# Performance work log

Measured on AMD Instinct MI355X. Metric: run time of the kernel, lower is better.

The kernel has to match this reference:

```python
import jax, jax.numpy as jnp
import numpy as np
import math

B, H, L = 8, 256, 4096
C = 1            # channels
D_STATE = 64
DD = D_STATE // 2  # d = 32
DT_MIN, DT_MAX = 1e-3, 1e-1


def setup_inputs() -> dict:
    key = jax.random.key(0)
    ks = jax.random.split(key, 6)
    u = jax.random.normal(ks[0], (B, H, L), dtype=jnp.float32)
    # analytic init matching the torch module
    h_scale = jnp.exp(jnp.arange(H, dtype=jnp.float32) / H * math.log(DT_MAX / DT_MIN))  # (H,)
    angles = jnp.arange(DD, dtype=jnp.float32) * jnp.float32(np.pi)                      # (DD,)
    theta = jnp.einsum('c,h,d->chd', jnp.ones((C,), jnp.float32), h_scale, angles)       # (C,H,DD)
    a = -jnp.broadcast_to(h_scale[None, :, None], (C, H, DD)).astype(jnp.float32)        # (C,H,DD)
    D = jax.random.normal(ks[1], (C, H), dtype=jnp.float32)
    b_p = jax.random.normal(ks[2], (C, H, DD), dtype=jnp.float32)
    c_p = jax.random.normal(ks[3], (C, H, DD), dtype=jnp.float32)
    x0 = jax.random.normal(ks[4], (C, H, DD), dtype=jnp.float32)
    return {"u": u, "theta": theta, "a": a, "D": D, "b_p": b_p, "c_p": c_p, "x0": x0}


def fft_conv(u, f):
    # u: (B,H,L), f: (C,H,L) -> (B,C,H,L) causal conv via zero-padded FFT
    l = u.shape[-1]
    n = 2 * l
    u_f = jnp.fft.rfft(u, n=n)          # (B,H,n//2+1)
    f_f = jnp.fft.rfft(f, n=n)          # (C,H,n//2+1)
    y_f = jnp.einsum('bhl,chl->bchl', u_f, f_f)
    return jnp.fft.irfft(y_f, n=n)[..., :l]


def reference(u, theta, a, D, b_p, c_p, x0):
    l = u.shape[-1]
    T = 1.0 / (l - 1)
    zk = T * jnp.arange(l, dtype=jnp.float32)            # (L,)
    zk4 = zk[None, None, :, None]                         # (1,1,L,1)
    ls = -jnp.abs(a) + 1j * theta                         # (C,H,DD) complex
    term_0 = (jnp.exp(ls * T) - 1.0) / ls                 # (C,H,DD)
    # base_term: (C,H,L,DD)
    base_term = (2.0 * term_0[:, :, None, :] * jnp.exp(ls[:, :, None, :] * zk4)).real
    q = b_p * c_p                                         # (C,H,DD)
    f = jnp.einsum('chd,chld->chl', q, base_term)         # (C,H,L)
    y = fft_conv(u, f)                                    # (B,C,H,L)
    y = y + jnp.einsum('bhl,ch->bchl', u, D)
    # initial-condition term
    cos_term = 2.0 * T * jnp.exp(-jnp.abs(a)[:, :, None, :] * zk4) * jnp.cos(theta[:, :, None, :] * zk4)
    init = jnp.einsum('chd,chld->chl', 2.0 * (c_p * x0), cos_term)  # (C,H,L)
    y = y + init[None]                                    # broadcast over batch
    b = y.shape[0]
    return y.reshape(b, -1, l)                            # (B, C*H, L)
```

## Files before the change

kernel.cpp:

```cpp
#include <hip/hip_runtime.h>

#define BB 8
#define HH 256
#define LL 4096
#define STR 72

typedef __attribute__((ext_vector_type(8))) short short8;
typedef __attribute__((ext_vector_type(4))) float f32x4;

static __device__ inline unsigned short f2bf(float x) {
    union { float f; unsigned u; } v; v.f = x;
    unsigned r = v.u + 0x7fffu + ((v.u >> 16) & 1u);
    return (unsigned short)(r >> 16);
}
static __device__ inline float bf2f(unsigned short us) {
    union { unsigned u; float f; } v; v.u = ((unsigned)us) << 16; return v.f;
}

#define CMUL(or_, oi_, ar_, ai_, br_, bi_) do { \
    float _tr = fmaf((ar_), (br_), -(ai_) * (bi_)); \
    float _ti = fmaf((ar_), (bi_), (ai_) * (br_)); \
    (or_) = _tr; (oi_) = _ti; } while (0)

__global__ __launch_bounds__(256, 4) void s4_fused_kernel(
    const float* __restrict__ u, const float* __restrict__ theta,
    const float* __restrict__ a, const float* __restrict__ Dp,
    const float* __restrict__ b_p, const float* __restrict__ c_p,
    const float* __restrict__ x0, float* __restrict__ out)
{
    const int tid = threadIdx.x;
    const int blk = blockIdx.x;
    const int hh  = blk >> 2;
    const int bp  = blk & 3;

    __shared__ __align__(16) short UsA[64 * STR];
    __shared__ __align__(16) short UsB[64 * STR];
    __shared__ __align__(16) short EQ[64 * STR];
    __shared__ __align__(16) float Seg[32 * 18];
    __shared__ float h_s[64];

    const int d    = tid & 31;
    const int kb   = tid >> 5;
    const int g    = tid >> 5;
    const int ln   = tid & 63;
    const int m0   = (tid >> 6) << 4;
    const int rowi = ln & 15;
    const int quad = ln >> 4;

    const float* up0 = u + ((((size_t)(bp * 2) * HH) + hh) << 12);
    const float* up1 = u + ((((size_t)(bp * 2 + 1) * HH) + hh) << 12);
    float4 v0[4];
    #pragma unroll
    for (int jj = 0; jj < 4; ++jj)
        v0[jj] = ((const float4*)up0)[tid + (jj << 8)];

    const float T = 1.0f / (LL - 1);
    const float lr = a[hh * 32 + d];
    const float li = theta[hh * 32 + d];
    float sn, cS;
    sincosf(li * T, &sn, &cS);
    const float er = expf(lr * T);
    const float Rr = er * cS, Ri = er * sn;
    const float den = lr * lr + li * li;
    const float t0r = ((Rr - 1.f) * lr + Ri * li) / den;
    const float t0i = (Ri * lr - (Rr - 1.f) * li) / den;
    const float qq  = b_p[hh * 32 + d] * c_p[hh * 32 + d];
    const float wre = 2.f * qq * t0r, wim = 2.f * qq * t0i;
    const float vv  = 4.f * T * c_p[hh * 32 + d] * x0[hh * 32 + d];
    const float Dh  = Dp[hh];

    float r2r, r2i, r4r, r4i, r8r, r8i, r16r, r16i, r32r, r32i;
    CMUL(r2r, r2i, Rr, Ri, Rr, Ri);
    CMUL(r4r, r4i, r2r, r2i, r2r, r2i);
    CMUL(r8r, r8i, r4r, r4i, r4r, r4i);
    CMUL(r16r, r16i, r8r, r8i, r8r, r8i);
    CMUL(r32r, r32i, r16r, r16i, r16r, r16i);

    {
        float pr = 1.f, pi = 0.f;
        if (kb & 1) CMUL(pr, pi, pr, pi, r8r, r8i);
        if (kb & 2) CMUL(pr, pi, pr, pi, r16r, r16i);
        if (kb & 4) CMUL(pr, pi, pr, pi, r32r, r32i);
        #pragma unroll
        for (int k8 = 0; k8 < 8; ++k8) {
            const int k = (kb << 3) + k8;
            EQ[k * STR + d]            = (short)f2bf(pr);
            EQ[k * STR + 32 + d]       = (short)f2bf(-pi);
            UsB[d * STR + (63 - k)]        = (short)f2bf(pr);
            UsB[(32 + d) * STR + (63 - k)] = (short)f2bf(pi);
            float hk = fmaf(wre, pr, -wim * pi);
            hk += __shfl_xor(hk, 1);
            hk += __shfl_xor(hk, 2);
            hk += __shfl_xor(hk, 4);
            hk += __shfl_xor(hk, 8);
            hk += __shfl_xor(hk, 16);
            if (d == 0) h_s[k] = hk;
            CMUL(pr, pi, pr, pi, Rr, Ri);
        }
    }

    float Ar, Ai, wrr, wri;
    CMUL(Ar, Ai, r32r, r32i, r32r, r32i);
    CMUL(wrr, wri, wre, wim, Rr, Ri);
    float S8r, S8i, S16r, S16i, S32r, S32i;
    {
        float b1r, b1i, b2r, b2i;
        CMUL(b1r, b1i, Ar, Ai, Ar, Ai);
        CMUL(b2r, b2i, b1r, b1i, b1r, b1i);
        CMUL(S8r, S8i, b2r, b2i, b2r, b2i);
        CMUL(S16r, S16i, S8r, S8i, S8r, S8i);
        CMUL(S32r, S32i, S16r, S16i, S16r, S16i);
    }
    __syncthreads();

    {
        const int t  = tid >> 2;
        const int tb = (tid & 3) << 4;
        #pragma unroll
        for (int gg = 0; gg < 4; ++gg) {
            const int tau0 = tb + (gg << 2);
            unsigned short e[4];
            #pragma unroll
            for (int i = 0; i < 4; ++i) {
                const int dt = t - (tau0 + i);
                e[i] = (dt >= 0) ? f2bf(h_s[dt]) : (unsigned short)0;
            }
            uint2 pk;
            pk.x = (unsigned)e[0] | ((unsigned)e[1] << 16);
            pk.y = (unsigned)e[2] | ((unsigned)e[3] << 16);
            *(uint2*)&UsA[t * STR + tau0] = pk;
        }
    }
    __syncthreads();

    short8 aH[2], aP[2], aR[2];
    #pragma unroll
    for (int kh = 0; kh < 2; ++kh) {
        const int off = (m0 + rowi) * STR + (kh << 5) + (quad << 3);
        aH[kh] = *(const short8*)&UsA[off];
        aP[kh] = *(const short8*)&UsB[off];
        aR[kh] = *(const short8*)&EQ[off];
    }
    __syncthreads();

    #pragma unroll
    for (int jj = 0; jj < 4; ++jj) {
        const int v  = tid + (jj << 8);
        const int c  = v >> 4;
        const int t0 = (v & 15) << 2;
        uint2 pk;
        pk.x = (unsigned)f2bf(v0[jj].x) | ((unsigned)f2bf(v0[jj].y) << 16);
        pk.y = (unsigned)f2bf(v0[jj].z) | ((unsigned)f2bf(v0[jj].w) << 16);
        *(uint2*)&UsA[c * STR + t0] = pk;
    }
    float4 v1[4];
    #pragma unroll
    for (int jj = 0; jj < 4; ++jj)
        v1[jj] = ((const float4*)up1)[tid + (jj << 8)];
    __syncthreads();

    #pragma unroll
    for (int it = 0; it < 2; ++it) {
        short* Us = it ? UsB : UsA;

        f32x4 accY[4], accE[4];
        #pragma unroll
        for (int nt = 0; nt < 4; ++nt) {
            accY[nt] = (f32x4){0.f, 0.f, 0.f, 0.f};
            accE[nt] = (f32x4){0.f, 0.f, 0.f, 0.f};
        }
        #pragma unroll
        for (int kh = 0; kh < 2; ++kh) {
            const int k0 = kh << 5;
            #pragma unroll
            for (int nt = 0; nt < 4; ++nt) {
                const short8 bU = *(const short8*)&Us[((nt << 4) + rowi) * STR + k0 + (quad << 3)];
                accY[nt] = __builtin_amdgcn_mfma_f32_16x16x32_bf16(aH[kh], bU, accY[nt], 0, 0, 0);
                accE[nt] = __builtin_amdgcn_mfma_f32_16x16x32_bf16(aP[kh], bU, accE[nt], 0, 0, 0);
            }
        }

        #pragma unroll
        for (int nt = 0; nt < 4; ++nt) {
            uint2 pk;
            pk.x = (unsigned)f2bf(accE[nt][0]) | ((unsigned)f2bf(accE[nt][1]) << 16);
            pk.y = (unsigned)f2bf(accE[nt][2]) | ((unsigned)f2bf(accE[nt][3]) << 16);
            *(uint2*)&EQ[((nt << 4) + rowi) * STR + m0 + (quad << 2)] = pk;
        }

        if (it == 0) {
            #pragma unroll
            for (int jj = 0; jj < 4; ++jj) {
                const int v  = tid + (jj << 8);
                const int c  = v >> 4;
                const int t0 = (v & 15) << 2;
                uint2 pk;
                pk.x = (unsigned)f2bf(v1[jj].x) | ((unsigned)f2bf(v1[jj].y) << 16);
                pk.y = (unsigned)f2bf(v1[jj].z) | ((unsigned)f2bf(v1[jj].w) << 16);
                *(uint2*)&UsB[c * STR + t0] = pk;
            }
        }
        __syncthreads();

        const int cb = g << 3;
        float Er[8], Ei[8];
        {
            float Sr = 0.f, Si = 0.f;
            #pragma unroll
            for (int i = 0; i < 8; ++i) {
                const int c = cb + i;
                Er[i] = bf2f((unsigned short)EQ[c * STR + d]);
                Ei[i] = bf2f((unsigned short)EQ[c * STR + 32 + d]);
                const float nr = fmaf(Ar, Sr, fmaf(-Ai, Si, Er[i]));
                const float ni = fmaf(Ar, Si, fmaf(Ai, Sr, Ei[i]));
                Sr = nr; Si = ni;
            }
            Seg[d * 18 + (g << 1)]     = Sr;
            Seg[d * 18 + (g << 1) + 1] = Si;
        }
        __syncthreads();

        {
            float offr = 0.f, offi = 0.f;
            #pragma unroll
            for (int gp = 0; gp < 7; ++gp) {
                const float2 sg = *(const float2*)&Seg[d * 18 + (gp << 1)];
                const float nr = fmaf(S8r, offr, fmaf(-S8i, offi, sg.x));
                const float ni = fmaf(S8r, offi, fmaf(S8i, offr, sg.y));
                const bool take = gp < g;
                offr = take ? nr : offr;
                offi = take ? ni : offi;
            }
            float Gr = vv, Gi = 0.f;
            if (g & 1) { float nr, ni; CMUL(nr, ni, Gr, Gi, S8r, S8i);   Gr = nr; Gi = ni; }
            if (g & 2) { float nr, ni; CMUL(nr, ni, Gr, Gi, S16r, S16i); Gr = nr; Gi = ni; }
            if (g & 4) { float nr, ni; CMUL(nr, ni, Gr, Gi, S32r, S32i); Gr = nr; Gi = ni; }
            float Sr = offr, Si = offi;
            #pragma unroll
            for (int i = 0; i < 8; ++i) {
                const int c = cb + i;
                const float Qr = fmaf(wrr, Sr, fmaf(-wri, Si, Gr));
                const float Qi = fmaf(wrr, Si, fmaf(wri, Sr, Gi));
                EQ[c * STR + d]      = (short)f2bf(Qr);
                EQ[c * STR + 32 + d] = (short)f2bf(Qi);
                const float nr = fmaf(Ar, Sr, fmaf(-Ai, Si, Er[i]));
                const float ni = fmaf(Ar, Si, fmaf(Ai, Sr, Ei[i]));
                Sr = nr; Si = ni;
                float nGr, nGi;
                CMUL(nGr, nGi, Ar, Ai, Gr, Gi);
                Gr = nGr; Gi = nGi;
            }
        }
        __syncthreads();

        #pragma unroll
        for (int kh = 0; kh < 2; ++kh) {
            const int k0 = kh << 5;
            #pragma unroll
            for (int nt = 0; nt < 4; ++nt) {
                const short8 bQ = *(const short8*)&EQ[((nt << 4) + rowi) * STR + k0 + (quad << 3)];
                accY[nt] = __builtin_amdgcn_mfma_f32_16x16x32_bf16(aR[kh], bQ, accY[nt], 0, 0, 0);
            }
        }

        float* op = out + ((((size_t)(bp * 2 + it) * HH) + hh) << 12);
        #pragma unroll
        for (int nt = 0; nt < 4; ++nt) {
            const int c    = (nt << 4) + rowi;
            const int toff = m0 + (quad << 2);
            const uint2 uu = *(const uint2*)&Us[c * STR + toff];
            float4 res;
            res.x = fmaf(Dh, bf2f((unsigned short)(uu.x & 0xffffu)), accY[nt][0]);
            res.y = fmaf(Dh, bf2f((unsigned short)(uu.x >> 16)),     accY[nt][1]);
            res.z = fmaf(Dh, bf2f((unsigned short)(uu.y & 0xffffu)), accY[nt][2]);
            res.w = fmaf(Dh, bf2f((unsigned short)(uu.y >> 16)),     accY[nt][3]);
            *(float4*)&op[c * 64 + toff] = res;
        }
        __syncthreads();
    }
}

extern "C" void kernel_launch(void* const* d_in, const int* in_sizes, int n_in,
                              void* d_out, int out_size, void* d_ws, size_t ws_size,
                              hipStream_t stream) {
    const float* u     = (const float*)d_in[0];
    const float* theta = (const float*)d_in[1];
    const float* a     = (const float*)d_in[2];
    const float* Dp    = (const float*)d_in[3];
    const float* b_p   = (const float*)d_in[4];
    const float* c_p   = (const float*)d_in[5];
    const float* x0    = (const float*)d_in[6];
    float* out = (float*)d_out;
    (void)d_ws; (void)ws_size;

    hipLaunchKernelGGL(s4_fused_kernel, dim3(HH * 4), dim3(256), 0, stream,
                       u, theta, a, Dp, b_p, c_p, x0, out);
}
```

Baseline: 101.7 us.

## Assign one batch per block and build Toeplitz fragment directly in registers

The grid grows from 1024 blocks handling two batches each to 2048 blocks handling one batch each. This removes the per-block loop and the second u prefetch. The Toeplitz A-fragment is now built in registers from a bf16 h vector kept in shared memory, rather than staged through a shared-memory matrix, which drops one LDS pass and two barriers. In exchange, each block still recomputes the per-h setup (powers, P and R matrices), so that setup work doubles across the grid, and the in-block overlap of the next batch's load goes away.

```diff
diff --git a/kernel.cpp b/kernel.cpp
--- a/kernel.cpp
+++ b/kernel.cpp
@@ -30,14 +30,14 @@
 {
     const int tid = threadIdx.x;
     const int blk = blockIdx.x;
-    const int hh  = blk >> 2;
-    const int bp  = blk & 3;
-
-    __shared__ __align__(16) short UsA[64 * STR];
-    __shared__ __align__(16) short UsB[64 * STR];
+    const int hh  = blk >> 3;
+    const int b   = blk & 7;
+
+    __shared__ __align__(16) short Us[64 * STR];
+    __shared__ __align__(16) short Pm[64 * STR];
     __shared__ __align__(16) short EQ[64 * STR];
     __shared__ __align__(16) float Seg[32 * 18];
-    __shared__ float h_s[64];
+    __shared__ unsigned short h_sb[64];
 
     const int d    = tid & 31;
     const int kb   = tid >> 5;
@@ -47,12 +47,11 @@
     const int rowi = ln & 15;
     const int quad = ln >> 4;
 
-    const float* up0 = u + ((((size_t)(bp * 2) * HH) + hh) << 12);
-    const float* up1 = u + ((((size_t)(bp * 2 + 1) * HH) + hh) << 12);
+    const float* up = u + ((((size_t)b * HH) + hh) << 12);
     float4 v0[4];
     #pragma unroll
     for (int jj = 0; jj < 4; ++jj)
-        v0[jj] = ((const float4*)up0)[tid + (jj << 8)];
+        v0[jj] = ((const float4*)up)[tid + (jj << 8)];
 
     const float T = 1.0f / (LL - 1);
     const float lr = a[hh * 32 + d];
@@ -86,15 +85,15 @@
             const int k = (kb << 3) + k8;
             EQ[k * STR + d]            = (short)f2bf(pr);
             EQ[k * STR + 32 + d]       = (short)f2bf(-pi);
-            UsB[d * STR + (63 - k)]        = (short)f2bf(pr);
-            UsB[(32 + d) * STR + (63 - k)] = (short)f2bf(pi);
+            Pm[d * STR + (63 - k)]        = (short)f2bf(pr);
+            Pm[(32 + d) * STR + (63 - k)] = (short)f2bf(pi);
             float hk = fmaf(wre, pr, -wim * pi);
             hk += __shfl_xor(hk, 1);
             hk += __shfl_xor(hk, 2);
             hk += __shfl_xor(hk, 4);
             hk += __shfl_xor(hk, 8);
             hk += __shfl_xor(hk, 16);
-            if (d == 0) h_s[k] = hk;
+            if (d == 0) h_sb[k] = f2bf(hk);
             CMUL(pr, pi, pr, pi, Rr, Ri);
         }
     }
@@ -113,35 +112,23 @@
     }
     __syncthreads();
 
-    {
-        const int t  = tid >> 2;
-        const int tb = (tid & 3) << 4;
-        #pragma unroll
-        for (int gg = 0; gg < 4; ++gg) {
-            const int tau0 = tb + (gg << 2);
-            unsigned short e[4];
-            #pragma unroll
-            for (int i = 0; i < 4; ++i) {
-                const int dt = t - (tau0 + i);
-                e[i] = (dt >= 0) ? f2bf(h_s[dt]) : (unsigned short)0;
-            }
-            uint2 pk;
-            pk.x = (unsigned)e[0] | ((unsigned)e[1] << 16);
-            pk.y = (unsigned)e[2] | ((unsigned)e[3] << 16);
-            *(uint2*)&UsA[t * STR + tau0] = pk;
-        }
-    }
-    __syncthreads();
-
     short8 aH[2], aP[2], aR[2];
     #pragma unroll
     for (int kh = 0; kh < 2; ++kh) {
         const int off = (m0 + rowi) * STR + (kh << 5) + (quad << 3);
-        aH[kh] = *(const short8*)&UsA[off];
-        aP[kh] = *(const short8*)&UsB[off];
+        aP[kh] = *(const short8*)&Pm[off];
         aR[kh] = *(const short8*)&EQ[off];
     }
-    __syncthreads();
+    #pragma unroll
+    for (int kh = 0; kh < 2; ++kh) {
+        short8 hv;
+        #pragma unroll
+        for (int j = 0; j < 8; ++j) {
+            const int dt = (m0 + rowi) - ((kh << 5) + (quad << 3) + j);
+            hv[j] = (dt >= 0) ? (short)h_sb[dt] : (short)0;
+        }
+        aH[kh] = hv;
+    }
 
     #pragma unroll
     for (int jj = 0; jj < 4; ++jj) {
@@ -151,132 +138,109 @@
         uint2 pk;
         pk.x = (unsigned)f2bf(v0[jj].x) | ((unsigned)f2bf(v0[jj].y) << 16);
         pk.y = (unsigned)f2bf(v0[jj].z) | ((unsigned)f2bf(v0[jj].w) << 16);
-        *(uint2*)&UsA[c * STR + t0] = pk;
-    }
-    float4 v1[4];
-    #pragma unroll
-    for (int jj = 0; jj < 4; ++jj)
-        v1[jj] = ((const float4*)up1)[tid + (jj << 8)];
-    __syncthreads();
-
-    #pragma unroll
-    for (int it = 0; it < 2; ++it) {
-        short* Us = it ? UsB : UsA;
-
-        f32x4 accY[4], accE[4];
+        *(uint2*)&Us[c * STR + t0] = pk;
+    }
+    __syncthreads();
+
+    f32x4 accY[4], accE[4];
+    #pragma unroll
+    for (int nt = 0; nt < 4; ++nt) {
+        accY[nt] = (f32x4){0.f, 0.f, 0.f, 0.f};
+        accE[nt] = (f32x4){0.f, 0.f, 0.f, 0.f};
+    }
+    #pragma unroll
+    for (int kh = 0; kh < 2; ++kh) {
+        const int k0 = kh << 5;
         #pragma unroll
         for (int nt = 0; nt < 4; ++nt) {
-            accY[nt] = (f32x4){0.f, 0.f, 0.f, 0.f};
-            accE[nt] = (f32x4){0.f, 0.f, 0.f, 0.f};
-        }
-        #pragma unroll
-        for (int kh = 0; kh < 2; ++kh) {
-            const int k0 = kh << 5;
-            #pragma unroll
-            for (int nt = 0; nt < 4; ++nt) {
-                const short8 bU = *(const short8*)&Us[((nt << 4) + rowi) * STR + k0 + (quad << 3)];
-                accY[nt] = __builtin_amdgcn_mfma_f32_16x16x32_bf16(aH[kh], bU, accY[nt], 0, 0, 0);
-                accE[nt] = __builtin_amdgcn_mfma_f32_16x16x32_bf16(aP[kh], bU, accE[nt], 0, 0, 0);
-            }
-        }
-
+            const short8 bU = *(const short8*)&Us[((nt << 4) + rowi) * STR + k0 + (quad << 3)];
+            accY[nt] = __builtin_amdgcn_mfma_f32_16x16x32_bf16(aH[kh], bU, accY[nt], 0, 0, 0);
+            accE[nt] = __builtin_amdgcn_mfma_f32_16x16x32_bf16(aP[kh], bU, accE[nt], 0, 0, 0);
+        }
+    }
+
+    #pragma unroll
+    for (int nt = 0; nt < 4; ++nt) {
+        uint2 pk;
+        pk.x = (unsigned)f2bf(accE[nt][0]) | ((unsigned)f2bf(accE[nt][1]) << 16);
+        pk.y = (unsigned)f2bf(accE[nt][2]) | ((unsigned)f2bf(accE[nt][3]) << 16);
+        *(uint2*)&EQ[((nt << 4) + rowi) * STR + m0 + (quad << 2)] = pk;
+    }
+    __syncthreads();
+
+    const int cb = g << 3;
+    float Er[8], Ei[8];
+    {
+        float Sr = 0.f, Si = 0.f;
+        #pragma unroll
+        for (int i = 0; i < 8; ++i) {
+            const int c = cb + i;
+            Er[i] = bf2f((unsigned short)EQ[c * STR + d]);
+            Ei[i] = bf2f((unsigned short)EQ[c * STR + 32 + d]);
+            const float nr = fmaf(Ar, Sr, fmaf(-Ai, Si, Er[i]));
+            const float ni = fmaf(Ar, Si, fmaf(Ai, Sr, Ei[i]));
+            Sr = nr; Si = ni;
+        }
+        Seg[d * 18 + (g << 1)]     = Sr;
+        Seg[d * 18 + (g << 1) + 1] = Si;
+    }
+    __syncthreads();
+
+    {
+        float offr = 0.f, offi = 0.f;
+        #pragma unroll
+        for (int gp = 0; gp < 7; ++gp) {
+            const float2 sg = *(const float2*)&Seg[d * 18 + (gp << 1)];
+            const float nr = fmaf(S8r, offr, fmaf(-S8i, offi, sg.x));
+            const float ni = fmaf(S8r, offi, fmaf(S8i, offr, sg.y));
+            const bool take = gp < g;
+            offr = take ? nr : offr;
+            offi = take ? ni : offi;
+        }
+        float Gr = vv, Gi = 0.f;
+        if (g & 1) { float nr, ni; CMUL(nr, ni, Gr, Gi, S8r, S8i);   Gr = nr; Gi = ni; }
+        if (g & 2) { float nr, ni; CMUL(nr, ni, Gr, Gi, S16r, S16i); Gr = nr; Gi = ni; }
+        if (g & 4) { float nr, ni; CMUL(nr, ni, Gr, Gi, S32r, S32i); Gr = nr; Gi = ni; }
+        float Sr = offr, Si = offi;
+        #pragma unroll
+        for (int i = 0; i < 8; ++i) {
+            const int c = cb + i;
+            const float Qr = fmaf(wrr, Sr, fmaf(-wri, Si, Gr));
+            const float Qi = fmaf(wrr, Si, fmaf(wri, Sr, Gi));
+            EQ[c * STR + d]      = (short)f2bf(Qr);
+            EQ[c * STR + 32 + d] = (short)f2bf(Qi);
+            const float nr = fmaf(Ar, Sr, fmaf(-Ai, Si, Er[i]));
+            const float ni = fmaf(Ar, Si, fmaf(Ai, Sr, Ei[i]));
+            Sr = nr; Si = ni;
+            float nGr, nGi;
+            CMUL(nGr, nGi, Ar, Ai, Gr, Gi);
+            Gr = nGr; Gi = nGi;
+        }
+    }
+    __syncthreads();
+
+    #pragma unroll
+    for (int kh = 0; kh < 2; ++kh) {
+        const int k0 = kh << 5;
         #pragma unroll
         for (int nt = 0; nt < 4; ++nt) {
-            uint2 pk;
-            pk.x = (unsigned)f2bf(accE[nt][0]) | ((unsigned)f2bf(accE[nt][1]) << 16);
-            pk.y = (unsigned)f2bf(accE[nt][2]) | ((unsigned)f2bf(accE[nt][3]) << 16);
-            *(uint2*)&EQ[((nt << 4) + rowi) * STR + m0 + (quad << 2)] = pk;
-        }
-
-        if (it == 0) {
-            #pragma unroll
-            for (int jj = 0; jj < 4; ++jj) {
-                const int v  = tid + (jj << 8);
-                const int c  = v >> 4;
-                const int t0 = (v & 15) << 2;
-                uint2 pk;
-                pk.x = (unsigned)f2bf(v1[jj].x) | ((unsigned)f2bf(v1[jj].y) << 16);
-                pk.y = (unsigned)f2bf(v1[jj].z) | ((unsigned)f2bf(v1[jj].w) << 16);
-                *(uint2*)&UsB[c * STR + t0] = pk;
-            }
-        }
-        __syncthreads();
-
-        const int cb = g << 3;
-        float Er[8], Ei[8];
-        {
-            float Sr = 0.f, Si = 0.f;
-            #pragma unroll
-            for (int i = 0; i < 8; ++i) {
-                const int c = cb + i;
-                Er[i] = bf2f((unsigned short)EQ[c * STR + d]);
-                Ei[i] = bf2f((unsigned short)EQ[c * STR + 32 + d]);
-                const float nr = fmaf(Ar, Sr, fmaf(-Ai, Si, Er[i]));
-                const float ni = fmaf(Ar, Si, fmaf(Ai, Sr, Ei[i]));
-                Sr = nr; Si = ni;
-            }
-            Seg[d * 18 + (g << 1)]     = Sr;
-            Seg[d * 18 + (g << 1) + 1] = Si;
-        }
-        __syncthreads();
-
-        {
-            float offr = 0.f, offi = 0.f;
-            #pragma unroll
-            for (int gp = 0; gp < 7; ++gp) {
-                const float2 sg = *(const float2*)&Seg[d * 18 + (gp << 1)];
-                const float nr = fmaf(S8r, offr, fmaf(-S8i, offi, sg.x));
-                const float ni = fmaf(S8r, offi, fmaf(S8i, offr, sg.y));
-                const bool take = gp < g;
-                offr = take ? nr : offr;
-                offi = take ? ni : offi;
-            }
-            float Gr = vv, Gi = 0.f;
-            if (g & 1) { float nr, ni; CMUL(nr, ni, Gr, Gi, S8r, S8i);   Gr = nr; Gi = ni; }
-            if (g & 2) { float nr, ni; CMUL(nr, ni, Gr, Gi, S16r, S16i); Gr = nr; Gi = ni; }
-            if (g & 4) { float nr, ni; CMUL(nr, ni, Gr, Gi, S32r, S32i); Gr = nr; Gi = ni; }
-            float Sr = offr, Si = offi;
-            #pragma unroll
-            for (int i = 0; i < 8; ++i) {
-                const int c = cb + i;
-                const float Qr = fmaf(wrr, Sr, fmaf(-wri, Si, Gr));
-                const float Qi = fmaf(wrr, Si, fmaf(wri, Sr, Gi));
-                EQ[c * STR + d]      = (short)f2bf(Qr);
-                EQ[c * STR + 32 + d] = (short)f2bf(Qi);
-                const float nr = fmaf(Ar, Sr, fmaf(-Ai, Si, Er[i]));
-                const float ni = fmaf(Ar, Si, fmaf(Ai, Sr, Ei[i]));
-                Sr = nr; Si = ni;
-                float nGr, nGi;
-                CMUL(nGr, nGi, Ar, Ai, Gr, Gi);
-                Gr = nGr; Gi = nGi;
-            }
-        }
-        __syncthreads();
-
-        #pragma unroll
-        for (int kh = 0; kh < 2; ++kh) {
-            const int k0 = kh << 5;
-            #pragma unroll
-            for (int nt = 0; nt < 4; ++nt) {
-                const short8 bQ = *(const short8*)&EQ[((nt << 4) + rowi) * STR + k0 + (quad << 3)];
-                accY[nt] = __builtin_amdgcn_mfma_f32_16x16x32_bf16(aR[kh], bQ, accY[nt], 0, 0, 0);
-            }
-        }
-
-        float* op = out + ((((size_t)(bp * 2 + it) * HH) + hh) << 12);
-        #pragma unroll
-        for (int nt = 0; nt < 4; ++nt) {
-            const int c    = (nt << 4) + rowi;
-            const int toff = m0 + (quad << 2);
-            const uint2 uu = *(const uint2*)&Us[c * STR + toff];
-            float4 res;
-            res.x = fmaf(Dh, bf2f((unsigned short)(uu.x & 0xffffu)), accY[nt][0]);
-            res.y = fmaf(Dh, bf2f((unsigned short)(uu.x >> 16)),     accY[nt][1]);
-            res.z = fmaf(Dh, bf2f((unsigned short)(uu.y & 0xffffu)), accY[nt][2]);
-            res.w = fmaf(Dh, bf2f((unsigned short)(uu.y >> 16)),     accY[nt][3]);
-            *(float4*)&op[c * 64 + toff] = res;
-        }
-        __syncthreads();
+            const short8 bQ = *(const short8*)&EQ[((nt << 4) + rowi) * STR + k0 + (quad << 3)];
+            accY[nt] = __builtin_amdgcn_mfma_f32_16x16x32_bf16(aR[kh], bQ, accY[nt], 0, 0, 0);
+        }
+    }
+
+    float* op = out + ((((size_t)b * HH) + hh) << 12);
+    #pragma unroll
+    for (int nt = 0; nt < 4; ++nt) {
+        const int c    = (nt << 4) + rowi;
+        const int toff = m0 + (quad << 2);
+        const uint2 uu = *(const uint2*)&Us[c * STR + toff];
+        float4 res;
+        res.x = fmaf(Dh, bf2f((unsigned short)(uu.x & 0xffffu)), accY[nt][0]);
+        res.y = fmaf(Dh, bf2f((unsigned short)(uu.x >> 16)),     accY[nt][1]);
+        res.z = fmaf(Dh, bf2f((unsigned short)(uu.y & 0xffffu)), accY[nt][2]);
+        res.w = fmaf(Dh, bf2f((unsigned short)(uu.y >> 16)),     accY[nt][3]);
+        *(float4*)&op[c * 64 + toff] = res;
     }
 }
 
@@ -293,6 +257,6 @@
     float* out = (float*)d_out;
     (void)d_ws; (void)ws_size;
 
-    hipLaunchKernelGGL(s4_fused_kernel, dim3(HH * 4), dim3(256), 0, stream,
+    hipLaunchKernelGGL(s4_fused_kernel, dim3(BB * HH), dim3(256), 0, stream,
                        u, theta, a, Dp, b_p, c_p, x0, out);
 }
```

After: 105.1 us. +3.3%, slower.
